# Optimization experiments

Hardware: AMD Instinct MI355X
Metric: run time of the kernel (lower is better)

The kernel has to match this reference:

```python
import jax, jax.numpy as jnp
import numpy as np

B, L, C, H = 2, 4096, 1024, 16
D = C // H
KERNEL_FROM_KN = lambda kn: int(np.sqrt(kn)) + 1


def setup_inputs() -> dict:
    key = jax.random.key(0)
    ks = jax.random.split(key, 4)
    s = 0.02
    kk = KERNEL_FROM_KN(144)  # 13
    return {
        "x": jax.random.normal(ks[0], (B, L, C), jnp.float32),
        "w_qkv": jax.random.normal(ks[1], (C, 3 * C), jnp.float32) * s,
        "b_qkv": jnp.zeros((3 * C,), jnp.float32),
        "rpb": jax.random.normal(ks[2], (H, 2 * kk - 1), jnp.float32) * s,
        "w_proj": jax.random.normal(ks[3], (C, C), jnp.float32) * s,
        "b_proj": jnp.zeros((C,), jnp.float32),
        "k_neighbors": 144,
    }


def reference(x, w_qkv, b_qkv, rpb, w_proj, b_proj, k_neighbors):
    kk = KERNEL_FROM_KN(k_neighbors)  # kernel size (13)
    scale = D ** -0.5
    qkv = (x @ w_qkv + b_qkv).reshape(B, L, 3, H, D).transpose(2, 0, 3, 1, 4)  # (3,B,H,L,D)
    q, k, v = qkv[0] * scale, qkv[1], qkv[2]
    pos = jnp.arange(L)
    # NATTEN window: centered, clamped so the full kernel fits inside [0, L)
    start = jnp.clip(pos - kk // 2, 0, L - kk)               # (L,)
    idx = start[:, None] + jnp.arange(kk)[None, :]           # (L,kk) key positions
    k_win = k[:, :, idx, :]                                  # (B,H,L,kk,D)
    v_win = v[:, :, idx, :]                                  # (B,H,L,kk,D)
    attn = jnp.einsum('bhld,bhlkd->bhlk', q, k_win)          # (B,H,L,kk)
    # relative-position bias index = key_pos - query_pos + (kk - 1) in [0, 2kk-2]
    bias_idx = idx - pos[:, None] + (kk - 1)                 # (L,kk)
    attn = attn + rpb[:, bias_idx][None]                     # broadcast over batch
    attn = jax.nn.softmax(attn, axis=-1)
    out = jnp.einsum('bhlk,bhlkd->bhld', attn, v_win)        # (B,H,L,D)
    out = out.transpose(0, 2, 1, 3).reshape(B, L, C)
    return out @ w_proj + b_proj
```

## Files before the change

kernel.cpp:

```cpp
#include <hip/hip_runtime.h>
#include <hip/hip_bf16.h>
#include <stdint.h>

typedef __bf16 bf16x8 __attribute__((ext_vector_type(8)));
typedef float floatx4 __attribute__((ext_vector_type(4)));

#define B_ 2
#define L_ 4096
#define C_ 1024
#define H_ 16
#define D_ 64
constexpr size_t TEN = (size_t)B_ * H_ * L_ * D_;

__device__ __forceinline__ float bf2f(unsigned short u) {
  union { unsigned int i; float f; } x; x.i = ((unsigned int)u) << 16; return x.f;
}
__device__ __forceinline__ unsigned short f2bf(float f) {
  union { float f; unsigned int i; } x; x.f = f;
  unsigned int i = x.i;
  return (unsigned short)((i + 0x7FFFu + ((i >> 16) & 1u)) >> 16);
}

__global__ __launch_bounds__(256) void cvt_f32_bf16_kernel(
    const float* __restrict__ in, unsigned short* __restrict__ out, int n) {
  int i = (blockIdx.x * 256 + threadIdx.x) * 8;
  if (i >= n) return;
  float4 a = *(const float4*)&in[i];
  float4 b = *(const float4*)&in[i + 4];
  union { uint4 u; unsigned short s[8]; } st;
  st.s[0] = f2bf(a.x); st.s[1] = f2bf(a.y); st.s[2] = f2bf(a.z); st.s[3] = f2bf(a.w);
  st.s[4] = f2bf(b.x); st.s[5] = f2bf(b.y); st.s[6] = f2bf(b.z); st.s[7] = f2bf(b.w);
  *(uint4*)&out[i] = st.u;
}

__global__ __launch_bounds__(256) void transpose_f32_bf16(
    const float* __restrict__ in, unsigned short* __restrict__ out,
    int R, int Ccols) {
  __shared__ float tile[64][65];
  const int bx = blockIdx.x * 64;
  const int by = blockIdx.y * 64;
  const int t = threadIdx.x;
  for (int i = t; i < 1024; i += 256) {
    int r = i >> 4, c4 = (i & 15) << 2;
    float4 v = *(const float4*)&in[(size_t)(by + r) * Ccols + bx + c4];
    tile[r][c4] = v.x; tile[r][c4 + 1] = v.y; tile[r][c4 + 2] = v.z; tile[r][c4 + 3] = v.w;
  }
  __syncthreads();
  for (int i = t; i < 512; i += 256) {
    int r = i >> 3, c8 = (i & 7) << 3;
    union { uint4 u; unsigned short s[8]; } st;
    #pragma unroll
    for (int j = 0; j < 8; ++j) st.s[j] = f2bf(tile[c8 + j][r]);
    *(uint4*)&out[(size_t)(bx + r) * R + by + c8] = st.u;
  }
}

template <int MODE>
__global__ __launch_bounds__(256) void gemm_bt_kernel(
    const unsigned short* __restrict__ A, const unsigned short* __restrict__ Bt,
    const float* __restrict__ bias, unsigned short* __restrict__ out_bf,
    float* __restrict__ out_f, int M, int N, int K, float qscale) {
  constexpr int BK = 64;
  constexpr int LDA = 72;
  __shared__ unsigned short a_sh[128 * LDA];
  __shared__ unsigned short b_sh[128 * LDA];

  const int t = threadIdx.x;
  const int m0 = blockIdx.y * 128;
  const int n0 = blockIdx.x * 128;
  const int wave = t >> 6, lane = t & 63;
  const int wr = wave >> 1, wc = wave & 1;
  const int lm = lane & 15, quad = lane >> 4;

  floatx4 acc[4][4];
  #pragma unroll
  for (int i = 0; i < 4; ++i)
    #pragma unroll
    for (int j = 0; j < 4; ++j) acc[i][j] = (floatx4)0.0f;

  for (int kt = 0; kt < K; kt += BK) {
    #pragma unroll
    for (int p = 0; p < 4; ++p) {
      int idx = (p * 256 + t) * 8;
      int r = idx >> 6, c = idx & 63;
      uint4 va = *(const uint4*)&A[(size_t)(m0 + r) * K + kt + c];
      *(uint4*)&a_sh[r * LDA + c] = va;
      uint4 vb = *(const uint4*)&Bt[(size_t)(n0 + r) * K + kt + c];
      *(uint4*)&b_sh[r * LDA + c] = vb;
    }
    __syncthreads();
    #pragma unroll
    for (int ks = 0; ks < BK; ks += 32) {
      bf16x8 af[4], bfr[4];
      #pragma unroll
      for (int i = 0; i < 4; ++i)
        af[i] = *(const bf16x8*)&a_sh[(wr * 64 + i * 16 + lm) * LDA + ks + quad * 8];
      #pragma unroll
      for (int j = 0; j < 4; ++j)
        bfr[j] = *(const bf16x8*)&b_sh[(wc * 64 + j * 16 + lm) * LDA + ks + quad * 8];
      #pragma unroll
      for (int i = 0; i < 4; ++i)
        #pragma unroll
        for (int j = 0; j < 4; ++j)
          acc[i][j] = __builtin_amdgcn_mfma_f32_16x16x32_bf16(af[i], bfr[j], acc[i][j], 0, 0, 0);
    }
    __syncthreads();
  }

  #pragma unroll
  for (int j = 0; j < 4; ++j) {
    int col = n0 + wc * 64 + j * 16 + lm;
    float bv = bias[col];
    if (MODE == 0) {
      int which = col >> 10;
      int rem = col & 1023;
      int h = rem >> 6, d = rem & 63;
      float mul = (which == 0) ? qscale : 1.0f;
      #pragma unroll
      for (int i = 0; i < 4; ++i)
        #pragma unroll
        for (int r = 0; r < 4; ++r) {
          int row = m0 + wr * 64 + i * 16 + quad * 4 + r;
          int b = row >> 12, l = row & (L_ - 1);
          float v = (acc[i][j][r] + bv) * mul;
          out_bf[(size_t)which * TEN + (((size_t)(b * H_ + h) * L_ + l) * D_ + d)] = f2bf(v);
        }
    } else {
      #pragma unroll
      for (int i = 0; i < 4; ++i)
        #pragma unroll
        for (int r = 0; r < 4; ++r) {
          int row = m0 + wr * 64 + i * 16 + quad * 4 + r;
          out_f[(size_t)row * N + col] = acc[i][j][r] + bv;
        }
    }
  }
}

constexpr int KKMAX = 63;
constexpr int TL = 128;
constexpr int LDK = 72;

__global__ __launch_bounds__(256) void natt_kernel(
    const unsigned short* __restrict__ qkv,
    const float* __restrict__ rpb,
    const int* __restrict__ knp,
    unsigned short* __restrict__ attn_out) {
  __shared__ unsigned short k_sh[(TL + KKMAX) * LDK];
  __shared__ unsigned short v_sh[(TL + KKMAX) * LDK];
  __shared__ float rpb_sh[2 * KKMAX + 1];

  const int bh = blockIdx.x;
  const int h = bh & (H_ - 1);
  const int b = bh >> 4;
  const int l0 = blockIdx.y * TL;
  const int t = threadIdx.x;

  int kn = knp[0];
  if (kn > 65536 || kn < 0) {
    union { int i; float f; } u; u.i = kn; kn = (int)u.f;
  }
  int rr = 1;
  while ((rr + 1) * (rr + 1) <= kn) ++rr;
  int kk = rr + 1;
  if (kk > KKMAX) kk = KKMAX;

  int base = l0 - kk / 2;
  if (base < 0) base = 0;
  if (base > L_ - kk) base = L_ - kk;
  int nrows = TL + kk;
  if (nrows > L_ - base) nrows = L_ - base;

  const unsigned short* kg = qkv + TEN + (size_t)bh * L_ * D_;
  const unsigned short* vg = qkv + 2 * TEN + (size_t)bh * L_ * D_;

  for (int i = t; i < nrows * 8; i += 256) {
    int row = i >> 3, c8 = (i & 7) << 3;
    uint4 kv = *(const uint4*)&kg[(size_t)(base + row) * D_ + c8];
    *(uint4*)&k_sh[row * LDK + c8] = kv;
    uint4 vv = *(const uint4*)&vg[(size_t)(base + row) * D_ + c8];
    *(uint4*)&v_sh[row * LDK + c8] = vv;
  }
  int nb = 2 * kk - 1;
  for (int i = t; i < nb; i += 256) rpb_sh[i] = rpb[h * nb + i];
  __syncthreads();

  const int qi = t >> 1, half = t & 1;
  const int l = l0 + qi;

  const unsigned short* qg = qkv + (size_t)bh * L_ * D_ + (size_t)l * D_ + half * 32;
  float qv[32];
  #pragma unroll
  for (int c = 0; c < 4; ++c) {
    union { uint4 u; unsigned short s[8]; } ld;
    ld.u = *(const uint4*)&qg[c * 8];
    #pragma unroll
    for (int j = 0; j < 8; ++j) qv[c * 8 + j] = bf2f(ld.s[j]);
  }

  int start = l - kk / 2;
  if (start < 0) start = 0;
  if (start > L_ - kk) start = L_ - kk;
  const int srow = start - base;
  const int boff = start - l + kk - 1;

  float m = -1e30f, lsum = 0.0f;
  float accv[32];
  #pragma unroll
  for (int d = 0; d < 32; ++d) accv[d] = 0.0f;

  for (int j = 0; j < kk; ++j) {
    const unsigned short* kr = &k_sh[(srow + j) * LDK + half * 32];
    float partial = 0.0f;
    #pragma unroll
    for (int c = 0; c < 4; ++c) {
      union { uint4 u; unsigned short s[8]; } ld;
      ld.u = *(const uint4*)&kr[c * 8];
      #pragma unroll
      for (int jj = 0; jj < 8; ++jj) partial += qv[c * 8 + jj] * bf2f(ld.s[jj]);
    }
    float s = partial + __shfl_xor(partial, 1) + rpb_sh[boff + j];
    float p;
    if (s > m) {
      float corr = __expf(m - s);
      lsum *= corr;
      #pragma unroll
      for (int d = 0; d < 32; ++d) accv[d] *= corr;
      m = s;
      p = 1.0f;
    } else {
      p = __expf(s - m);
    }
    lsum += p;
    const unsigned short* vr = &v_sh[(srow + j) * LDK + half * 32];
    #pragma unroll
    for (int c = 0; c < 4; ++c) {
      union { uint4 u; unsigned short s[8]; } ld;
      ld.u = *(const uint4*)&vr[c * 8];
      #pragma unroll
      for (int jj = 0; jj < 8; ++jj) accv[c * 8 + jj] += p * bf2f(ld.s[jj]);
    }
  }
  float inv = 1.0f / lsum;
  unsigned short* og = attn_out + ((size_t)(b * L_ + l) * C_ + h * D_ + half * 32);
  #pragma unroll
  for (int c = 0; c < 4; ++c) {
    union { uint4 u; unsigned short s[8]; } st;
    #pragma unroll
    for (int jj = 0; jj < 8; ++jj) st.s[jj] = f2bf(accv[c * 8 + jj] * inv);
    *(uint4*)&og[c * 8] = st.u;
  }
}

extern "C" void kernel_launch(void* const* d_in, const int* in_sizes, int n_in,
                              void* d_out, int out_size, void* d_ws, size_t ws_size,
                              hipStream_t stream) {
  const float* x      = (const float*)d_in[0];
  const float* w_qkv  = (const float*)d_in[1];
  const float* b_qkv  = (const float*)d_in[2];
  const float* rpb    = (const float*)d_in[3];
  const float* w_proj = (const float*)d_in[4];
  const float* b_proj = (const float*)d_in[5];
  const int* kn       = (const int*)d_in[6];
  float* out          = (float*)d_out;

  unsigned short* ws      = (unsigned short*)d_ws;
  unsigned short* wT_qkv  = ws;
  unsigned short* wT_proj = wT_qkv + (size_t)3072 * 1024;
  unsigned short* x_bf    = wT_proj + (size_t)1024 * 1024;
  unsigned short* qkv_ws  = x_bf + (size_t)8192 * 1024;
  unsigned short* attn_ws = qkv_ws + 3 * TEN;

  cvt_f32_bf16_kernel<<<(8192 * 1024) / (256 * 8), 256, 0, stream>>>(x, x_bf, 8192 * 1024);
  transpose_f32_bf16<<<dim3(3072 / 64, 1024 / 64), 256, 0, stream>>>(w_qkv, wT_qkv, 1024, 3072);
  transpose_f32_bf16<<<dim3(1024 / 64, 1024 / 64), 256, 0, stream>>>(w_proj, wT_proj, 1024, 1024);
  gemm_bt_kernel<0><<<dim3(3072 / 128, 8192 / 128), 256, 0, stream>>>(
      x_bf, wT_qkv, b_qkv, qkv_ws, nullptr, 8192, 3072, 1024, 0.125f);
  natt_kernel<<<dim3(B_ * H_, L_ / TL), 256, 0, stream>>>(qkv_ws, rpb, kn, attn_ws);
  gemm_bt_kernel<1><<<dim3(1024 / 128, 8192 / 128), 256, 0, stream>>>(
      attn_ws, wT_proj, b_proj, nullptr, out, 8192, 1024, 1024, 1.0f);
}
```

Before: 226.5 us.

## Use direct global-to-LDS loads in GEMM and two-pass softmax for small windows

The GEMM tile loads now use global_load_lds to copy 16-byte chunks straight from global memory into shared memory, so the data no longer passes through registers. To fit that instruction's contiguous per-wave layout, the LDS padding is dropped (stride 64 instead of 72), which may add bank conflicts on the MFMA fragment reads. Separately, the neighborhood attention kernel adds a fully unrolled path for windows of up to 16 keys. It computes all scores first, then the max, then exponentials and the V accumulation, removing the branchy online-softmax rescaling of the 32 accumulators.

```diff
diff --git a/kernel.cpp b/kernel.cpp
--- a/kernel.cpp
+++ b/kernel.cpp
@@ -19,6 +19,12 @@
   union { float f; unsigned int i; } x; x.f = f;
   unsigned int i = x.i;
   return (unsigned short)((i + 0x7FFFu + ((i >> 16) & 1u)) >> 16);
+}
+
+__device__ __forceinline__ void g2lds16(const unsigned short* g, unsigned short* l) {
+  __builtin_amdgcn_global_load_lds((__attribute__((address_space(1))) void*)g,
+                                   (__attribute__((address_space(3))) void*)l,
+                                   16, 0, 0);
 }
 
 __global__ __launch_bounds__(256) void cvt_f32_bf16_kernel(
@@ -61,9 +67,8 @@
     const float* __restrict__ bias, unsigned short* __restrict__ out_bf,
     float* __restrict__ out_f, int M, int N, int K, float qscale) {
   constexpr int BK = 64;
-  constexpr int LDA = 72;
-  __shared__ unsigned short a_sh[128 * LDA];
-  __shared__ unsigned short b_sh[128 * LDA];
+  __shared__ unsigned short a_sh[128 * BK];
+  __shared__ unsigned short b_sh[128 * BK];
 
   const int t = threadIdx.x;
   const int m0 = blockIdx.y * 128;
@@ -78,15 +83,18 @@
     #pragma unroll
     for (int j = 0; j < 4; ++j) acc[i][j] = (floatx4)0.0f;
 
+  const int r0 = (t * 8) >> 6;
+  const int c0 = (t * 8) & 63;
+  const unsigned short* gA = &A[(size_t)(m0 + r0) * K + c0];
+  const unsigned short* gB = &Bt[(size_t)(n0 + r0) * K + c0];
+  unsigned short* lA = &a_sh[(size_t)(t & ~63) * 8];
+  unsigned short* lB = &b_sh[(size_t)(t & ~63) * 8];
+
   for (int kt = 0; kt < K; kt += BK) {
     #pragma unroll
     for (int p = 0; p < 4; ++p) {
-      int idx = (p * 256 + t) * 8;
-      int r = idx >> 6, c = idx & 63;
-      uint4 va = *(const uint4*)&A[(size_t)(m0 + r) * K + kt + c];
-      *(uint4*)&a_sh[r * LDA + c] = va;
-      uint4 vb = *(const uint4*)&Bt[(size_t)(n0 + r) * K + kt + c];
-      *(uint4*)&b_sh[r * LDA + c] = vb;
+      g2lds16(gA + (size_t)(p * 32) * K + kt, lA + p * 2048);
+      g2lds16(gB + (size_t)(p * 32) * K + kt, lB + p * 2048);
     }
     __syncthreads();
     #pragma unroll
@@ -94,10 +102,10 @@
       bf16x8 af[4], bfr[4];
       #pragma unroll
       for (int i = 0; i < 4; ++i)
-        af[i] = *(const bf16x8*)&a_sh[(wr * 64 + i * 16 + lm) * LDA + ks + quad * 8];
+        af[i] = *(const bf16x8*)&a_sh[(wr * 64 + i * 16 + lm) * BK + ks + quad * 8];
       #pragma unroll
       for (int j = 0; j < 4; ++j)
-        bfr[j] = *(const bf16x8*)&b_sh[(wc * 64 + j * 16 + lm) * LDA + ks + quad * 8];
+        bfr[j] = *(const bf16x8*)&b_sh[(wc * 64 + j * 16 + lm) * BK + ks + quad * 8];
       #pragma unroll
       for (int i = 0; i < 4; ++i)
         #pragma unroll
@@ -204,43 +212,82 @@
   const int srow = start - base;
   const int boff = start - l + kk - 1;
 
-  float m = -1e30f, lsum = 0.0f;
   float accv[32];
   #pragma unroll
   for (int d = 0; d < 32; ++d) accv[d] = 0.0f;
-
-  for (int j = 0; j < kk; ++j) {
-    const unsigned short* kr = &k_sh[(srow + j) * LDK + half * 32];
-    float partial = 0.0f;
-    #pragma unroll
-    for (int c = 0; c < 4; ++c) {
-      union { uint4 u; unsigned short s[8]; } ld;
-      ld.u = *(const uint4*)&kr[c * 8];
-      #pragma unroll
-      for (int jj = 0; jj < 8; ++jj) partial += qv[c * 8 + jj] * bf2f(ld.s[jj]);
-    }
-    float s = partial + __shfl_xor(partial, 1) + rpb_sh[boff + j];
-    float p;
-    if (s > m) {
-      float corr = __expf(m - s);
-      lsum *= corr;
-      #pragma unroll
-      for (int d = 0; d < 32; ++d) accv[d] *= corr;
-      m = s;
-      p = 1.0f;
-    } else {
-      p = __expf(s - m);
-    }
-    lsum += p;
-    const unsigned short* vr = &v_sh[(srow + j) * LDK + half * 32];
-    #pragma unroll
-    for (int c = 0; c < 4; ++c) {
-      union { uint4 u; unsigned short s[8]; } ld;
-      ld.u = *(const uint4*)&vr[c * 8];
-      #pragma unroll
-      for (int jj = 0; jj < 8; ++jj) accv[c * 8 + jj] += p * bf2f(ld.s[jj]);
-    }
-  }
+  float lsum = 0.0f;
+
+  if (kk <= 16) {
+    float sarr[16];
+    float mx = -1e30f;
+    #pragma unroll
+    for (int j = 0; j < 16; ++j) {
+      if (j < kk) {
+        const unsigned short* kr = &k_sh[(srow + j) * LDK + half * 32];
+        float partial = 0.0f;
+        #pragma unroll
+        for (int c = 0; c < 4; ++c) {
+          union { uint4 u; unsigned short s[8]; } ld;
+          ld.u = *(const uint4*)&kr[c * 8];
+          #pragma unroll
+          for (int jj = 0; jj < 8; ++jj) partial += qv[c * 8 + jj] * bf2f(ld.s[jj]);
+        }
+        float s = partial + __shfl_xor(partial, 1) + rpb_sh[boff + j];
+        sarr[j] = s;
+        mx = fmaxf(mx, s);
+      }
+    }
+    #pragma unroll
+    for (int j = 0; j < 16; ++j) {
+      if (j < kk) {
+        float p = __expf(sarr[j] - mx);
+        lsum += p;
+        const unsigned short* vr = &v_sh[(srow + j) * LDK + half * 32];
+        #pragma unroll
+        for (int c = 0; c < 4; ++c) {
+          union { uint4 u; unsigned short s[8]; } ld;
+          ld.u = *(const uint4*)&vr[c * 8];
+          #pragma unroll
+          for (int jj = 0; jj < 8; ++jj) accv[c * 8 + jj] += p * bf2f(ld.s[jj]);
+        }
+      }
+    }
+  } else {
+    float m = -1e30f;
+    for (int j = 0; j < kk; ++j) {
+      const unsigned short* kr = &k_sh[(srow + j) * LDK + half * 32];
+      float partial = 0.0f;
+      #pragma unroll
+      for (int c = 0; c < 4; ++c) {
+        union { uint4 u; unsigned short s[8]; } ld;
+        ld.u = *(const uint4*)&kr[c * 8];
+        #pragma unroll
+        for (int jj = 0; jj < 8; ++jj) partial += qv[c * 8 + jj] * bf2f(ld.s[jj]);
+      }
+      float s = partial + __shfl_xor(partial, 1) + rpb_sh[boff + j];
+      float p;
+      if (s > m) {
+        float corr = __expf(m - s);
+        lsum *= corr;
+        #pragma unroll
+        for (int d = 0; d < 32; ++d) accv[d] *= corr;
+        m = s;
+        p = 1.0f;
+      } else {
+        p = __expf(s - m);
+      }
+      lsum += p;
+      const unsigned short* vr = &v_sh[(srow + j) * LDK + half * 32];
+      #pragma unroll
+      for (int c = 0; c < 4; ++c) {
+        union { uint4 u; unsigned short s[8]; } ld;
+        ld.u = *(const uint4*)&vr[c * 8];
+        #pragma unroll
+        for (int jj = 0; jj < 8; ++jj) accv[c * 8 + jj] += p * bf2f(ld.s[jj]);
+      }
+    }
+  }
+
   float inv = 1.0f / lsum;
   unsigned short* og = attn_out + ((size_t)(b * L_ + l) * C_ + h * D_ + half * 32);
   #pragma unroll
```

Measured after the change: 239.2 us. 1.06x slower.
